# Kernel optimization log

Hardware: AMD Instinct MI355X
Metric: run time of the kernel (lower is better)

## Reference

```python
import jax, jax.numpy as jnp
import numpy as np

# ---- static config ----
H, W = 60, 60
WS = 7          # window size (square)
SS = 3          # shift size
DIM = 256
NH = 8
HD = DIM // NH
N = WS * WS     # tokens per window = 49
HP = (H // WS + 1) * WS  # 63 (padded, matches __init__ mask construction)
WP = (W // WS + 1) * WS  # 63
NW = (HP // WS) * (WP // WS)  # 81 windows
EPS = 1e-5


def _rel_pos_index():
    coords = np.stack(np.meshgrid(np.arange(WS), np.arange(WS), indexing='ij'))  # (2,WS,WS)
    cf = coords.reshape(2, -1)                      # (2, N)
    rel = cf[:, :, None] - cf[:, None, :]           # (2, N, N)
    rel = rel.transpose(1, 2, 0).astype(np.int64)   # (N, N, 2)
    rel[..., 0] += WS - 1
    rel[..., 1] += WS - 1
    rel[..., 0] *= 2 * WS - 1
    return rel.sum(-1)                              # (N, N) in [0, 169)


def _attn_mask():
    img = np.zeros((HP, WP), dtype=np.float32)
    cnt = 0
    for hs in (slice(0, -WS), slice(-WS, -SS), slice(-SS, None)):
        for ws_ in (slice(0, -WS), slice(-WS, -SS), slice(-SS, None)):
            img[hs, ws_] = cnt
            cnt += 1
    mw = img.reshape(HP // WS, WS, WP // WS, WS).transpose(0, 2, 1, 3).reshape(-1, N)  # (NW, N)
    diff = mw[:, None, :] - mw[:, :, None]          # (NW, N, N)
    return np.where(diff != 0, -100.0, 0.0).astype(np.float32)


REL_IDX = _rel_pos_index()
ATTN_MASK = _attn_mask()


def layer_norm(x, g, b):
    mu = jnp.mean(x, axis=-1, keepdims=True)
    var = jnp.mean(jnp.square(x - mu), axis=-1, keepdims=True)
    return (x - mu) * jax.lax.rsqrt(var + EPS) * g + b


def setup_inputs() -> dict:
    key = jax.random.key(0)
    ks = jax.random.split(key, 8)
    B = 24
    std = 0.02
    return {
        'x': jax.random.normal(ks[0], (B, H * W, DIM), jnp.float32),
        'g1': jnp.ones((DIM,), jnp.float32),
        'b1': jnp.zeros((DIM,), jnp.float32),
        'w_qkv': jax.random.normal(ks[1], (DIM, 3 * DIM), jnp.float32) * std,
        'b_qkv': jnp.zeros((3 * DIM,), jnp.float32),
        'rel_bias_table': jax.random.normal(ks[2], ((2 * WS - 1) ** 2, NH), jnp.float32) * std,
        'w_proj': jax.random.normal(ks[3], (DIM, DIM), jnp.float32) * std,
        'b_proj': jnp.zeros((DIM,), jnp.float32),
        'g2': jnp.ones((DIM,), jnp.float32),
        'b2': jnp.zeros((DIM,), jnp.float32),
        'w_fc1': jax.random.normal(ks[4], (DIM, 4 * DIM), jnp.float32) * std,
        'b_fc1': jnp.zeros((4 * DIM,), jnp.float32),
        'w_fc2': jax.random.normal(ks[5], (4 * DIM, DIM), jnp.float32) * std,
        'b_fc2': jnp.zeros((DIM,), jnp.float32),
    }


def _swin_block(x, g1, b1, w_qkv, b_qkv, rel_bias_table, w_proj, b_proj,
                g2, b2, w_fc1, b_fc1, w_fc2, b_fc2):
    B, L, C = x.shape
    shortcut = x
    x = layer_norm(x, g1, b1).reshape(B, H, W, C)
    # pad to (HP, WP)
    x = jnp.pad(x, ((0, 0), (0, HP - H), (0, WP - W), (0, 0)))
    # cyclic shift
    x = jnp.roll(x, (-SS, -SS), axis=(1, 2))
    # window partition -> (B*NW, N, C)
    xw = x.reshape(B, HP // WS, WS, WP // WS, WS, C).transpose(0, 1, 3, 2, 4, 5)
    xw = xw.reshape(B * NW, N, C)
    # attention
    qkv = (xw @ w_qkv + b_qkv).reshape(B * NW, N, 3, NH, HD).transpose(2, 0, 3, 1, 4)
    q, k, v = qkv[0], qkv[1], qkv[2]            # (B*NW, NH, N, HD)
    q = q * (HD ** -0.5)
    attn = jnp.einsum('whnd,whmd->whnm', q, k)  # (B*NW, NH, N, N)
    rel_bias = rel_bias_table[jnp.asarray(REL_IDX)]          # (N, N, NH)
    attn = attn + rel_bias.transpose(2, 0, 1)[None]
    mask = jnp.asarray(ATTN_MASK)                            # (NW, N, N)
    attn = attn.reshape(B, NW, NH, N, N) + mask[None, :, None]
    attn = jax.nn.softmax(attn.reshape(B * NW, NH, N, N), axis=-1)
    out = jnp.einsum('whnm,whmd->whnd', attn, v)             # (B*NW, NH, N, HD)
    out = out.transpose(0, 2, 1, 3).reshape(B * NW, N, C)
    out = out @ w_proj + b_proj
    # window reverse -> (B, HP, WP, C)
    out = out.reshape(B, HP // WS, WP // WS, WS, WS, C).transpose(0, 1, 3, 2, 4, 5)
    out = out.reshape(B, HP, WP, C)
    # reverse shift, unpad
    out = jnp.roll(out, (SS, SS), axis=(1, 2))[:, :H, :W, :].reshape(B, L, C)
    x = shortcut + out
    # MLP
    y = layer_norm(x, g2, b2)
    y = jax.nn.gelu(y @ w_fc1 + b_fc1, approximate=False) @ w_fc2 + b_fc2
    return x + y


def reference(x, g1, b1, w_qkv, b_qkv, rel_bias_table, w_proj, b_proj,
              g2, b2, w_fc1, b_fc1, w_fc2, b_fc2):
    return _swin_block(x, g1, b1, w_qkv, b_qkv, rel_bias_table, w_proj, b_proj,
                       g2, b2, w_fc1, b_fc1, w_fc2, b_fc2)
```

## Files before the change

kernel.cpp:

```cpp
#include <hip/hip_runtime.h>
#include <hip/hip_bf16.h>
#include <math.h>


typedef _Float16 half8 __attribute__((ext_vector_type(8)));
typedef _Float16 half4_t __attribute__((ext_vector_type(4)));
typedef float f32x4 __attribute__((ext_vector_type(4)));

#define GLDS16(gp, lp)                                                    \
  __builtin_amdgcn_global_load_lds(                                      \
      (__attribute__((address_space(1))) const void*)(gp),               \
      (__attribute__((address_space(3))) void*)(lp), 16, 0, 0)

__device__ __forceinline__ float wave_reduce_sum(float v) {
  v += __shfl_xor(v, 1);
  v += __shfl_xor(v, 2);
  v += __shfl_xor(v, 4);
  v += __shfl_xor(v, 8);
  v += __shfl_xor(v, 16);
  v += __shfl_xor(v, 32);
  return v;
}

__global__ __launch_bounds__(256) void prep_weights(
    const float* __restrict__ wqkv, const float* __restrict__ wproj,
    const float* __restrict__ wfc1, const float* __restrict__ wfc2,
    _Float16* __restrict__ oqkv, _Float16* __restrict__ oproj,
    _Float16* __restrict__ ofc1, _Float16* __restrict__ ofc2)
{
  int idx = blockIdx.x * 256 + threadIdx.x;
  if (idx < 196608) {
    int n = idx / 256, k = idx % 256;
    oqkv[idx] = (_Float16)wqkv[k * 768 + n];
  } else if (idx < 262144) {
    int i = idx - 196608; int n = i / 256, k = i % 256;
    oproj[i] = (_Float16)wproj[k * 256 + n];
  } else if (idx < 524288) {
    int i = idx - 262144; int n = i / 256, k = i % 256;
    ofc1[i] = (_Float16)wfc1[k * 1024 + n];
  } else {
    int i = idx - 524288; int n = i / 1024, k = i % 1024;
    ofc2[i] = (_Float16)wfc2[k * 256 + n];
  }
}

__global__ __launch_bounds__(256) void prep_cb(
    const float* __restrict__ rbt, _Float16* __restrict__ cbt)
{
  int idx = blockIdx.x * 256 + threadIdx.x;
  int m = idx & 63, n = (idx >> 6) & 63;
  int hc = idx >> 12; int h = hc & 7, c = hc >> 3;
  float v;
  if (n < 49 && m < 49) {
    int i1 = n / 7, j1 = n % 7, i2 = m / 7, j2 = m % 7;
    float bias = rbt[((i1 - i2 + 6) * 13 + (j1 - j2 + 6)) * 8 + h];
    int rh1 = (c & 2) ? (i1 < 4 ? 1 : 2) : 0;
    int rh2 = (c & 2) ? (i2 < 4 ? 1 : 2) : 0;
    int rw1 = (c & 1) ? (j1 < 4 ? 1 : 2) : 0;
    int rw2 = (c & 1) ? (j2 < 4 ? 1 : 2) : 0;
    v = bias + (((rh1 != rh2) || (rw1 != rw2)) ? -100.f : 0.f);
  } else {
    v = -60000.f;
  }
  cbt[idx] = (_Float16)v;
}

__global__ __launch_bounds__(256) void ln1_window_kernel(
    const float* __restrict__ x, const float* __restrict__ g,
    const float* __restrict__ bta, _Float16* __restrict__ xw,
    int row0, int rows_c)
{
  int lrow = blockIdx.x * 4 + (threadIdx.x >> 6);
  if (lrow >= rows_c) return;
  int row = row0 + lrow;
  int lane = threadIdx.x & 63;
  int bw = row / 49, n = row - bw * 49;
  int b = bw / 81, win = bw - b * 81;
  int wh = win / 9, ww = win - wh * 9;
  int i = n / 7, j = n - i * 7;
  int sh = wh * 7 + i + 3; if (sh >= 63) sh -= 63;
  int sw = ww * 7 + j + 3; if (sw >= 63) sw -= 63;
  bool valid = (sh < 60) && (sw < 60);
  float4 v = make_float4(0.f, 0.f, 0.f, 0.f);
  if (valid)
    v = reinterpret_cast<const float4*>(x + ((size_t)b * 3600 + sh * 60 + sw) * 256)[lane];
  float s = v.x + v.y + v.z + v.w;
  s = wave_reduce_sum(s);
  float mu = s * (1.f / 256.f);
  float dx = v.x - mu, dy = v.y - mu, dz = v.z - mu, dw = v.w - mu;
  float q = dx * dx + dy * dy + dz * dz + dw * dw;
  q = wave_reduce_sum(q);
  float rs = rsqrtf(q * (1.f / 256.f) + 1e-5f);
  float4 gv = reinterpret_cast<const float4*>(g)[lane];
  float4 bv = reinterpret_cast<const float4*>(bta)[lane];
  union { _Float16 h[4]; uint2 u; } pk;
  if (valid) {
    pk.h[0] = (_Float16)(dx * rs * gv.x + bv.x);
    pk.h[1] = (_Float16)(dy * rs * gv.y + bv.y);
    pk.h[2] = (_Float16)(dz * rs * gv.z + bv.z);
    pk.h[3] = (_Float16)(dw * rs * gv.w + bv.w);
  } else {
    pk.h[0] = pk.h[1] = pk.h[2] = pk.h[3] = (_Float16)0.f;
  }
  *reinterpret_cast<uint2*>(xw + (size_t)lrow * 256 + lane * 4) = pk.u;
}

__global__ __launch_bounds__(256, 2) void gemm_kernel(
    const _Float16* __restrict__ A, const _Float16* __restrict__ Bt,
    const float* __restrict__ bias, const float* __restrict__ resid,
    void* __restrict__ out, int M, int N, int K, int mode, int row0)
{
  __shared__ __align__(16) _Float16 lds[2][2][8192];
  const int tid = threadIdx.x;
  const int n0 = blockIdx.x * 128, m0 = blockIdx.y * 128;
  const int wv = tid >> 6, ln = tid & 63;
  const int wm = (wv >> 1) * 64, wn = (wv & 1) * 64;
  const int quad = ln >> 4, l16 = ln & 15;

  const int rl = ln >> 3;
  const int gseg = ((ln & 7) ^ rl) << 3;
  const _Float16* gA[4]; const _Float16* gB[4];
#pragma unroll
  for (int s = 0; s < 4; s++) {
    int r = wv * 32 + s * 8 + rl;
    int gm = m0 + r; if (gm >= M) gm = M - 1;
    gA[s] = A + (size_t)gm * K + gseg;
    gB[s] = Bt + (size_t)(n0 + r) * K + gseg;
  }

  int offA[2][4], offB[2][4];
#pragma unroll
  for (int i = 0; i < 4; i++) {
    int ra = wm + i * 16 + l16;
    int rb = wn + i * 16 + l16;
    int sw0 = l16 & 7;
#pragma unroll
    for (int ks = 0; ks < 2; ks++) {
      offA[ks][i] = ra * 64 + (((ks * 4 + quad) ^ sw0) << 3);
      offB[ks][i] = rb * 64 + (((ks * 4 + quad) ^ sw0) << 3);
    }
  }

  f32x4 acc[4][4];
#pragma unroll
  for (int i = 0; i < 4; i++)
#pragma unroll
    for (int j = 0; j < 4; j++) acc[i][j] = (f32x4)0.f;

#define STAGE(buf, koff)                                                   \
  {                                                                        \
    _Float16* la = &lds[buf][0][wv * 2048];                                \
    _Float16* lb = &lds[buf][1][wv * 2048];                                \
    GLDS16(gA[0] + (koff), la);        GLDS16(gB[0] + (koff), lb);         \
    GLDS16(gA[1] + (koff), la + 512);  GLDS16(gB[1] + (koff), lb + 512);   \
    GLDS16(gA[2] + (koff), la + 1024); GLDS16(gB[2] + (koff), lb + 1024);  \
    GLDS16(gA[3] + (koff), la + 1536); GLDS16(gB[3] + (koff), lb + 1536);  \
  }

  const int nt = K >> 6;
  STAGE(0, 0);
  __syncthreads();
  for (int t = 0; t < nt; t++) {
    const int cur = t & 1;
    half8 a0[4], b0[4], a1[4], b1[4];
#pragma unroll
    for (int i = 0; i < 4; i++) {
      a0[i] = *reinterpret_cast<const half8*>(&lds[cur][0][offA[0][i]]);
      a1[i] = *reinterpret_cast<const half8*>(&lds[cur][0][offA[1][i]]);
      b0[i] = *reinterpret_cast<const half8*>(&lds[cur][1][offB[0][i]]);
      b1[i] = *reinterpret_cast<const half8*>(&lds[cur][1][offB[1][i]]);
    }
    if (t + 1 < nt) STAGE(cur ^ 1, (t + 1) << 6);
#pragma unroll
    for (int i = 0; i < 4; i++)
#pragma unroll
      for (int j = 0; j < 4; j++)
        acc[i][j] = __builtin_amdgcn_mfma_f32_16x16x32_f16(b0[j], a0[i], acc[i][j], 0, 0, 0);
#pragma unroll
    for (int i = 0; i < 4; i++)
#pragma unroll
      for (int j = 0; j < 4; j++)
        acc[i][j] = __builtin_amdgcn_mfma_f32_16x16x32_f16(b1[j], a1[i], acc[i][j], 0, 0, 0);
    __syncthreads();
  }
#undef STAGE

  f32x4 bias4[4];
#pragma unroll
  for (int j = 0; j < 4; j++)
    bias4[j] = *reinterpret_cast<const f32x4*>(bias + n0 + wn + j * 16 + quad * 4);

#pragma unroll
  for (int i = 0; i < 4; i++) {
    int gm = m0 + wm + i * 16 + l16;
    if (gm >= M) continue;
    if (mode == 0) {
      _Float16* op = reinterpret_cast<_Float16*>(out) + (size_t)gm * N + n0 + wn;
#pragma unroll
      for (int j = 0; j < 4; j++) {
        float sc = (n0 + wn + j * 16) < 256 ? 0.17677669529663687f : 1.f;
        half4_t o4;
#pragma unroll
        for (int r = 0; r < 4; r++)
          o4[r] = (_Float16)((acc[i][j][r] + bias4[j][r]) * sc);
        *reinterpret_cast<half4_t*>(op + j * 16 + quad * 4) = o4;
      }
    } else {
      int gmg = gm + row0;
      int bw = gmg / 49, nn = gmg - bw * 49;
      int bidx = bw / 81, win = bw - bidx * 81;
      int wh = win / 9, wwn = win - wh * 9;
      int ii = nn / 7, jj = nn - ii * 7;
      int sh = wh * 7 + ii + 3; if (sh >= 63) sh -= 63;
      int sw = wwn * 7 + jj + 3; if (sw >= 63) sw -= 63;
      if (sh < 60 && sw < 60) {
        size_t o = ((size_t)bidx * 3600 + sh * 60 + sw) * 256 + n0 + wn;
        float* op = reinterpret_cast<float*>(out) + o;
        const float* rp = resid + o;
#pragma unroll
        for (int j = 0; j < 4; j++) {
          f32x4 rv = *reinterpret_cast<const f32x4*>(rp + j * 16 + quad * 4);
          f32x4 v = acc[i][j] + bias4[j] + rv;
          *reinterpret_cast<f32x4*>(op + j * 16 + quad * 4) = v;
        }
      }
    }
  }
}

__global__ __launch_bounds__(256, 1) void fused_mlp_kernel(
    const float* __restrict__ X, const _Float16* __restrict__ W1t,
    const float* __restrict__ B1v, const _Float16* __restrict__ W2t,
    const float* __restrict__ B2v, const float* __restrict__ g,
    const float* __restrict__ bt, float* __restrict__ out, int M)
{
  __shared__ __align__(16) _Float16 Alds[128 * 256];
  __shared__ __align__(16) _Float16 Hlds[128 * 128];
  const int tid = threadIdx.x;
  const int wv = tid >> 6, ln = tid & 63;
  const int quad = ln >> 4, l16 = ln & 15;
  const int m0 = blockIdx.x * 128;
  const int wm = (wv >> 1) * 64;
  const int wn = (wv & 1) * 64;
  const int wn2 = (wv & 1) * 128;

  {
    float4 gv = reinterpret_cast<const float4*>(g)[ln];
    float4 bv = reinterpret_cast<const float4*>(bt)[ln];
    int seg = ln >> 1;
    for (int rr = 0; rr < 32; rr++) {
      int lr = wv * 32 + rr;
      int gr = m0 + lr; if (gr >= M) gr = M - 1;
      float4 v = reinterpret_cast<const float4*>(X + (size_t)gr * 256)[ln];
      float s = wave_reduce_sum(v.x + v.y + v.z + v.w);
      float mu = s * (1.f / 256.f);
      float dx = v.x - mu, dy = v.y - mu, dz = v.z - mu, dw = v.w - mu;
      float q = wave_reduce_sum(dx * dx + dy * dy + dz * dz + dw * dw);
      float rs = rsqrtf(q * (1.f / 256.f) + 1e-5f);
      union { _Float16 h[4]; uint2 u; } pk;
      pk.h[0] = (_Float16)(dx * rs * gv.x + bv.x);
      pk.h[1] = (_Float16)(dy * rs * gv.y + bv.y);
      pk.h[2] = (_Float16)(dz * rs * gv.z + bv.z);
      pk.h[3] = (_Float16)(dw * rs * gv.w + bv.w);
      *reinterpret_cast<uint2*>(
          &Alds[lr * 256 + ((seg ^ (lr & 31)) << 3) + (ln & 1) * 4]) = pk.u;
    }
  }

  f32x4 acc[4][8];
  {
    f32x4 b2q[8];
#pragma unroll
    for (int j = 0; j < 8; j++)
      b2q[j] = *reinterpret_cast<const f32x4*>(B2v + wn2 + j * 16 + quad * 4);
#pragma unroll
    for (int i = 0; i < 4; i++) {
      int gr = m0 + wm + i * 16 + l16; if (gr >= M) gr = M - 1;
      const float* xp = X + (size_t)gr * 256 + wn2;
#pragma unroll
      for (int j = 0; j < 8; j++)
        acc[i][j] = *reinterpret_cast<const f32x4*>(xp + j * 16 + quad * 4) + b2q[j];
    }
  }
  __syncthreads();

  for (int n1 = 0; n1 < 8; n1++) {
    f32x4 acch[4][4];
#pragma unroll
    for (int i = 0; i < 4; i++)
#pragma unroll
      for (int j = 0; j < 4; j++) acch[i][j] = (f32x4)0.f;
    for (int t = 0; t < 4; t++) {
#pragma unroll
      for (int ks = 0; ks < 2; ks++) {
        half8 bf[4], af[4];
#pragma unroll
        for (int j = 0; j < 4; j++)
          bf[j] = *reinterpret_cast<const half8*>(
              W1t + (size_t)(n1 * 128 + wn + j * 16 + l16) * 256 + t * 64 + ks * 32 + quad * 8);
#pragma unroll
        for (int i = 0; i < 4; i++) {
          int ra = wm + i * 16 + l16;
          af[i] = *reinterpret_cast<const half8*>(
              &Alds[ra * 256 + (((t * 8 + ks * 4 + quad) ^ (ra & 31)) << 3)]);
        }
#pragma unroll
        for (int i = 0; i < 4; i++)
#pragma unroll
          for (int j = 0; j < 4; j++)
            acch[i][j] = __builtin_amdgcn_mfma_f32_16x16x32_f16(bf[j], af[i], acch[i][j], 0, 0, 0);
      }
    }
    __syncthreads();
    {
      f32x4 b1q[4];
#pragma unroll
      for (int j = 0; j < 4; j++)
        b1q[j] = *reinterpret_cast<const f32x4*>(B1v + n1 * 128 + wn + j * 16 + quad * 4);
#pragma unroll
      for (int i = 0; i < 4; i++) {
        int mrow = wm + i * 16 + l16;
#pragma unroll
        for (int j = 0; j < 4; j++) {
          int c = wn + j * 16 + quad * 4;
          half4_t o4;
#pragma unroll
          for (int r = 0; r < 4; r++) {
            float v = acch[i][j][r] + b1q[j][r];
            v = 0.5f * v * (1.f + erff(v * 0.70710678118654752f));
            o4[r] = (_Float16)v;
          }
          *reinterpret_cast<half4_t*>(
              &Hlds[mrow * 128 + (((c >> 3) ^ (mrow & 15)) << 3) + (quad & 1) * 4]) = o4;
        }
      }
    }
    __syncthreads();
#pragma unroll
    for (int t2 = 0; t2 < 2; t2++) {
#pragma unroll
      for (int ks = 0; ks < 2; ks++) {
        half8 hf[4], b2f[8];
#pragma unroll
        for (int i = 0; i < 4; i++) {
          int mh = wm + i * 16 + l16;
          hf[i] = *reinterpret_cast<const half8*>(
              &Hlds[mh * 128 + (((t2 * 8 + ks * 4 + quad) ^ (mh & 15)) << 3)]);
        }
#pragma unroll
        for (int j = 0; j < 8; j++)
          b2f[j] = *reinterpret_cast<const half8*>(
              W2t + (size_t)(wn2 + j * 16 + l16) * 1024 + n1 * 128 + t2 * 64 + ks * 32 + quad * 8);
#pragma unroll
        for (int i = 0; i < 4; i++)
#pragma unroll
          for (int j = 0; j < 8; j++)
            acc[i][j] = __builtin_amdgcn_mfma_f32_16x16x32_f16(b2f[j], hf[i], acc[i][j], 0, 0, 0);
      }
    }
  }

#pragma unroll
  for (int i = 0; i < 4; i++) {
    int gm = m0 + wm + i * 16 + l16;
    if (gm >= M) continue;
    float* op = out + (size_t)gm * 256 + wn2;
#pragma unroll
    for (int j = 0; j < 8; j++)
      *reinterpret_cast<f32x4*>(op + j * 16 + quad * 4) = acc[i][j];
  }
}

__global__ __launch_bounds__(64) void attn_mfma(
    const _Float16* __restrict__ qkv, const _Float16* __restrict__ cbt,
    _Float16* __restrict__ outp)
{
  __shared__ __align__(16) _Float16 VT[32][72];
  __shared__ __align__(16) _Float16 Ps[64][72];
  const int bwh = blockIdx.x;
  const int bw = bwh >> 3, h = bwh & 7;
  const int win = bw % 81;
  const int wh = win / 9, ww = win - wh * 9;
  const int cls = ((wh == 8) ? 2 : 0) | ((ww == 8) ? 1 : 0);
  const int lane = threadIdx.x;
  const int quad = lane >> 4, l16 = lane & 15;

  for (int e = lane; e < 480; e += 64) {
    int d = e / 15, m = 49 + e % 15;
    VT[d][m] = (_Float16)0.f;
  }
  const size_t vbase = (size_t)bw * 49 * 768 + 512 + h * 32;
  for (int e = lane; e < 1568; e += 64) {
    int m = e >> 5, d = e & 31;
    VT[d][m] = qkv[vbase + (size_t)m * 768 + d];
  }

  const _Float16* qb = qkv + (size_t)bw * 49 * 768 + h * 32 + quad * 8;
  half8 kf[4], qf[4];
  const half8 hz = (half8)(_Float16)0.f;
#pragma unroll
  for (int t = 0; t < 4; t++) {
    int row = t * 16 + l16;
    int rc = row < 49 ? row : 48;
    half8 kv = *reinterpret_cast<const half8*>(qb + 256 + (size_t)rc * 768);
    half8 qv = *reinterpret_cast<const half8*>(qb + (size_t)rc * 768);
    kf[t] = row < 49 ? kv : hz;
    qf[t] = row < 49 ? qv : hz;
  }

  f32x4 S[4][4];
#pragma unroll
  for (int mt = 0; mt < 4; mt++)
#pragma unroll
    for (int nt = 0; nt < 4; nt++) S[mt][nt] = (f32x4)0.f;
#pragma unroll
  for (int mt = 0; mt < 4; mt++)
#pragma unroll
    for (int nt = 0; nt < 4; nt++)
      S[mt][nt] = __builtin_amdgcn_mfma_f32_16x16x32_f16(kf[mt], qf[nt], S[mt][nt], 0, 0, 0);

  const _Float16* cbp = cbt + (((size_t)cls * 8 + h) << 12);
#pragma unroll
  for (int nt = 0; nt < 4; nt++) {
    int n = nt * 16 + l16;
#pragma unroll
    for (int mt = 0; mt < 4; mt++) {
      half4_t cb4 = *reinterpret_cast<const half4_t*>(cbp + n * 64 + mt * 16 + quad * 4);
#pragma unroll
      for (int r = 0; r < 4; r++) S[mt][nt][r] += (float)cb4[r];
    }
  }

  float inv[4];
#pragma unroll
  for (int nt = 0; nt < 4; nt++) {
    float mx = -3.0e38f;
#pragma unroll
    for (int mt = 0; mt < 4; mt++)
#pragma unroll
      for (int r = 0; r < 4; r++) mx = fmaxf(mx, S[mt][nt][r]);
    mx = fmaxf(mx, __shfl_xor(mx, 16));
    mx = fmaxf(mx, __shfl_xor(mx, 32));
    float sm = 0.f;
#pragma unroll
    for (int mt = 0; mt < 4; mt++)
#pragma unroll
      for (int r = 0; r < 4; r++) {
        float e = __expf(S[mt][nt][r] - mx);
        S[mt][nt][r] = e;
        sm += e;
      }
    sm += __shfl_xor(sm, 16);
    sm += __shfl_xor(sm, 32);
    inv[nt] = 1.f / sm;
  }

#pragma unroll
  for (int nt = 0; nt < 4; nt++) {
#pragma unroll
    for (int mt = 0; mt < 4; mt++) {
      half4_t p;
#pragma unroll
      for (int r = 0; r < 4; r++) p[r] = (_Float16)(S[mt][nt][r] * inv[nt]);
      *reinterpret_cast<half4_t*>(&Ps[nt * 16 + l16][mt * 16 + quad * 4]) = p;
    }
  }
  __syncthreads();

  f32x4 O[2][4];
#pragma unroll
  for (int dt = 0; dt < 2; dt++)
#pragma unroll
    for (int nt = 0; nt < 4; nt++) O[dt][nt] = (f32x4)0.f;
#pragma unroll
  for (int ks = 0; ks < 2; ks++) {
    half8 va[2], pb[4];
#pragma unroll
    for (int dt = 0; dt < 2; dt++)
      va[dt] = *reinterpret_cast<const half8*>(&VT[dt * 16 + l16][ks * 32 + quad * 8]);
#pragma unroll
    for (int nt = 0; nt < 4; nt++)
      pb[nt] = *reinterpret_cast<const half8*>(&Ps[nt * 16 + l16][ks * 32 + quad * 8]);
#pragma unroll
    for (int dt = 0; dt < 2; dt++)
#pragma unroll
      for (int nt = 0; nt < 4; nt++)
        O[dt][nt] = __builtin_amdgcn_mfma_f32_16x16x32_f16(va[dt], pb[nt], O[dt][nt], 0, 0, 0);
  }

#pragma unroll
  for (int nt = 0; nt < 4; nt++) {
    int n = nt * 16 + l16;
    if (n < 49) {
#pragma unroll
      for (int dt = 0; dt < 2; dt++) {
        half4_t o4;
#pragma unroll
        for (int r = 0; r < 4; r++) o4[r] = (_Float16)O[dt][nt][r];
        *reinterpret_cast<half4_t*>(
            outp + ((size_t)bw * 49 + n) * 256 + h * 32 + dt * 16 + quad * 4) = o4;
      }
    }
  }
}

extern "C" void kernel_launch(void* const* d_in, const int* in_sizes, int n_in,
                              void* d_out, int out_size, void* d_ws, size_t ws_size,
                              hipStream_t stream) {
  const float* x      = (const float*)d_in[0];
  const float* g1     = (const float*)d_in[1];
  const float* b1     = (const float*)d_in[2];
  const float* w_qkv  = (const float*)d_in[3];
  const float* b_qkv  = (const float*)d_in[4];
  const float* rbt    = (const float*)d_in[5];
  const float* w_proj = (const float*)d_in[6];
  const float* b_proj = (const float*)d_in[7];
  const float* g2     = (const float*)d_in[8];
  const float* b2     = (const float*)d_in[9];
  const float* w_fc1  = (const float*)d_in[10];
  const float* b_fc1  = (const float*)d_in[11];
  const float* w_fc2  = (const float*)d_in[12];
  const float* b_fc2  = (const float*)d_in[13];
  float* outp = (float*)d_out;

  char* ws = (char*)d_ws;
  _Float16* wqkvT  = (_Float16*)(ws + 0);
  _Float16* wprojT = (_Float16*)(ws + 393216);
  _Float16* wfc1T  = (_Float16*)(ws + 524288);
  _Float16* wfc2T  = (_Float16*)(ws + 1048576);
  _Float16* cbt    = (_Float16*)(ws + 1572864);
  const size_t WB = 1835008;

  const int cand[8] = {24, 12, 8, 6, 4, 3, 2, 1};
  int cb = 1;
  for (int ci = 0; ci < 8; ci++) {
    size_t need = WB + (size_t)cand[ci] * (2032128u + 6096384u);
    if (ws_size >= need) { cb = cand[ci]; break; }
  }
  const int nch = 24 / cb;

  _Float16* r1 = (_Float16*)(ws + WB);
  _Float16* r2 = (_Float16*)(ws + WB + (size_t)cb * 2032128u);

  prep_weights<<<3072, 256, 0, stream>>>(w_qkv, w_proj, w_fc1, w_fc2,
                                         wqkvT, wprojT, wfc1T, wfc2T);
  prep_cb<<<512, 256, 0, stream>>>(rbt, cbt);

  for (int c = 0; c < nch; c++) {
    const int b0 = c * cb;
    const int rows_att = cb * 81 * 49;
    const int row0_att = b0 * 81 * 49;
    const int rows_mlp = cb * 3600;
    const int row0_mlp = b0 * 3600;

    ln1_window_kernel<<<(rows_att + 3) / 4, 256, 0, stream>>>(
        x, g1, b1, r1, row0_att, rows_att);
    {
      dim3 g(6, (rows_att + 127) / 128);
      gemm_kernel<<<g, 256, 0, stream>>>(r1, wqkvT, b_qkv, nullptr, r2,
                                         rows_att, 768, 256, 0, 0);
    }
    attn_mfma<<<cb * 81 * 8, 64, 0, stream>>>(r2, cbt, r1);
    {
      dim3 g(2, (rows_att + 127) / 128);
      gemm_kernel<<<g, 256, 0, stream>>>(r1, wprojT, b_proj, x, outp,
                                         rows_att, 256, 256, 1, row0_att);
    }
    {
      float* od = outp + (size_t)row0_mlp * 256;
      fused_mlp_kernel<<<(rows_mlp + 127) / 128, 256, 0, stream>>>(
          od, wfc1T, b_fc1, wfc2T, b_fc2, g2, b2, od, rows_mlp);
    }
  }
}
```

Before: 753.9 us.

## Shrink fused MLP row tile to 64 and double-buffer hidden LDS tile

The fused LayerNorm+MLP kernel now processes 64 rows per block instead of 128. Each of the four waves owns a 32-column slice of the hidden chunk and a 64-column slice of the output. The hidden activation buffer is double-buffered, which removes one __syncthreads per chunk, and smaller LDS and register use allow two blocks per CU (launch bounds 256,2). The trade-off is that each block reloads W1/W2 fragments from global memory for half as many rows, so weight traffic per output row doubles, in exchange for more occupancy and more blocks.

```diff
diff --git a/kernel.cpp b/kernel.cpp
--- a/kernel.cpp
+++ b/kernel.cpp
@@ -228,28 +228,27 @@
   }
 }
 
-__global__ __launch_bounds__(256, 1) void fused_mlp_kernel(
+__global__ __launch_bounds__(256, 2) void fused_mlp_kernel(
     const float* __restrict__ X, const _Float16* __restrict__ W1t,
     const float* __restrict__ B1v, const _Float16* __restrict__ W2t,
     const float* __restrict__ B2v, const float* __restrict__ g,
     const float* __restrict__ bt, float* __restrict__ out, int M)
 {
-  __shared__ __align__(16) _Float16 Alds[128 * 256];
-  __shared__ __align__(16) _Float16 Hlds[128 * 128];
+  __shared__ __align__(16) _Float16 Alds[64 * 256];
+  __shared__ __align__(16) _Float16 Hlds[2][64 * 128];
   const int tid = threadIdx.x;
   const int wv = tid >> 6, ln = tid & 63;
   const int quad = ln >> 4, l16 = ln & 15;
-  const int m0 = blockIdx.x * 128;
-  const int wm = (wv >> 1) * 64;
-  const int wn = (wv & 1) * 64;
-  const int wn2 = (wv & 1) * 128;
+  const int m0 = blockIdx.x * 64;
+  const int wn1 = wv * 32;
+  const int wn2 = wv * 64;
 
   {
     float4 gv = reinterpret_cast<const float4*>(g)[ln];
     float4 bv = reinterpret_cast<const float4*>(bt)[ln];
-    int seg = ln >> 1;
-    for (int rr = 0; rr < 32; rr++) {
-      int lr = wv * 32 + rr;
+    const int seg = ln >> 1;
+    for (int rr = 0; rr < 16; rr++) {
+      int lr = wv * 16 + rr;
       int gr = m0 + lr; if (gr >= M) gr = M - 1;
       float4 v = reinterpret_cast<const float4*>(X + (size_t)gr * 256)[ln];
       float s = wave_reduce_sum(v.x + v.y + v.z + v.w);
@@ -267,62 +266,61 @@
     }
   }
 
-  f32x4 acc[4][8];
+  f32x4 acc[4][4];
   {
-    f32x4 b2q[8];
-#pragma unroll
-    for (int j = 0; j < 8; j++)
+    f32x4 b2q[4];
+#pragma unroll
+    for (int j = 0; j < 4; j++)
       b2q[j] = *reinterpret_cast<const f32x4*>(B2v + wn2 + j * 16 + quad * 4);
 #pragma unroll
     for (int i = 0; i < 4; i++) {
-      int gr = m0 + wm + i * 16 + l16; if (gr >= M) gr = M - 1;
+      int gr = m0 + i * 16 + l16; if (gr >= M) gr = M - 1;
       const float* xp = X + (size_t)gr * 256 + wn2;
 #pragma unroll
-      for (int j = 0; j < 8; j++)
+      for (int j = 0; j < 4; j++)
         acc[i][j] = *reinterpret_cast<const f32x4*>(xp + j * 16 + quad * 4) + b2q[j];
     }
   }
   __syncthreads();
 
-  for (int n1 = 0; n1 < 8; n1++) {
-    f32x4 acch[4][4];
+  for (int n1c = 0; n1c < 8; n1c++) {
+    f32x4 acch[4][2];
 #pragma unroll
     for (int i = 0; i < 4; i++)
 #pragma unroll
-      for (int j = 0; j < 4; j++) acch[i][j] = (f32x4)0.f;
-    for (int t = 0; t < 4; t++) {
-#pragma unroll
-      for (int ks = 0; ks < 2; ks++) {
-        half8 bf[4], af[4];
-#pragma unroll
-        for (int j = 0; j < 4; j++)
-          bf[j] = *reinterpret_cast<const half8*>(
-              W1t + (size_t)(n1 * 128 + wn + j * 16 + l16) * 256 + t * 64 + ks * 32 + quad * 8);
-#pragma unroll
-        for (int i = 0; i < 4; i++) {
-          int ra = wm + i * 16 + l16;
-          af[i] = *reinterpret_cast<const half8*>(
-              &Alds[ra * 256 + (((t * 8 + ks * 4 + quad) ^ (ra & 31)) << 3)]);
-        }
-#pragma unroll
-        for (int i = 0; i < 4; i++)
-#pragma unroll
-          for (int j = 0; j < 4; j++)
-            acch[i][j] = __builtin_amdgcn_mfma_f32_16x16x32_f16(bf[j], af[i], acch[i][j], 0, 0, 0);
-      }
-    }
-    __syncthreads();
+      for (int j = 0; j < 2; j++) acch[i][j] = (f32x4)0.f;
+    const _Float16* w1p = W1t + (size_t)(n1c * 128 + wn1) * 256;
+#pragma unroll
+    for (int st = 0; st < 8; st++) {
+      half8 bf[2], af[4];
+#pragma unroll
+      for (int j = 0; j < 2; j++)
+        bf[j] = *reinterpret_cast<const half8*>(
+            w1p + (size_t)(j * 16 + l16) * 256 + st * 32 + quad * 8);
+#pragma unroll
+      for (int i = 0; i < 4; i++) {
+        int ra = i * 16 + l16;
+        af[i] = *reinterpret_cast<const half8*>(
+            &Alds[ra * 256 + (((st * 4 + quad) ^ (ra & 31)) << 3)]);
+      }
+#pragma unroll
+      for (int i = 0; i < 4; i++)
+#pragma unroll
+        for (int j = 0; j < 2; j++)
+          acch[i][j] = __builtin_amdgcn_mfma_f32_16x16x32_f16(bf[j], af[i], acch[i][j], 0, 0, 0);
+    }
+    _Float16* hb = &Hlds[n1c & 1][0];
     {
-      f32x4 b1q[4];
-#pragma unroll
-      for (int j = 0; j < 4; j++)
-        b1q[j] = *reinterpret_cast<const f32x4*>(B1v + n1 * 128 + wn + j * 16 + quad * 4);
+      f32x4 b1q[2];
+#pragma unroll
+      for (int j = 0; j < 2; j++)
+        b1q[j] = *reinterpret_cast<const f32x4*>(B1v + n1c * 128 + wn1 + j * 16 + quad * 4);
 #pragma unroll
       for (int i = 0; i < 4; i++) {
-        int mrow = wm + i * 16 + l16;
-#pragma unroll
-        for (int j = 0; j < 4; j++) {
-          int c = wn + j * 16 + quad * 4;
+        int m = i * 16 + l16;
+#pragma unroll
+        for (int j = 0; j < 2; j++) {
+          int n = wn1 + j * 16 + quad * 4;
           half4_t o4;
 #pragma unroll
           for (int r = 0; r < 4; r++) {
@@ -331,42 +329,40 @@
             o4[r] = (_Float16)v;
           }
           *reinterpret_cast<half4_t*>(
-              &Hlds[mrow * 128 + (((c >> 3) ^ (mrow & 15)) << 3) + (quad & 1) * 4]) = o4;
+              &hb[m * 128 + (((n >> 3) ^ (m & 15)) << 3) + (quad & 1) * 4]) = o4;
         }
       }
     }
     __syncthreads();
-#pragma unroll
-    for (int t2 = 0; t2 < 2; t2++) {
-#pragma unroll
-      for (int ks = 0; ks < 2; ks++) {
-        half8 hf[4], b2f[8];
-#pragma unroll
-        for (int i = 0; i < 4; i++) {
-          int mh = wm + i * 16 + l16;
-          hf[i] = *reinterpret_cast<const half8*>(
-              &Hlds[mh * 128 + (((t2 * 8 + ks * 4 + quad) ^ (mh & 15)) << 3)]);
-        }
-#pragma unroll
-        for (int j = 0; j < 8; j++)
-          b2f[j] = *reinterpret_cast<const half8*>(
-              W2t + (size_t)(wn2 + j * 16 + l16) * 1024 + n1 * 128 + t2 * 64 + ks * 32 + quad * 8);
-#pragma unroll
-        for (int i = 0; i < 4; i++)
-#pragma unroll
-          for (int j = 0; j < 8; j++)
-            acc[i][j] = __builtin_amdgcn_mfma_f32_16x16x32_f16(b2f[j], hf[i], acc[i][j], 0, 0, 0);
-      }
+    const _Float16* w2p = W2t + (size_t)wn2 * 1024 + n1c * 128;
+#pragma unroll
+    for (int p = 0; p < 4; p++) {
+      half8 hf[4], b2f[4];
+#pragma unroll
+      for (int j = 0; j < 4; j++)
+        b2f[j] = *reinterpret_cast<const half8*>(
+            w2p + (size_t)(j * 16 + l16) * 1024 + p * 32 + quad * 8);
+#pragma unroll
+      for (int i = 0; i < 4; i++) {
+        int mh = i * 16 + l16;
+        hf[i] = *reinterpret_cast<const half8*>(
+            &hb[mh * 128 + (((p * 4 + quad) ^ (mh & 15)) << 3)]);
+      }
+#pragma unroll
+      for (int i = 0; i < 4; i++)
+#pragma unroll
+        for (int j = 0; j < 4; j++)
+          acc[i][j] = __builtin_amdgcn_mfma_f32_16x16x32_f16(b2f[j], hf[i], acc[i][j], 0, 0, 0);
     }
   }
 
 #pragma unroll
   for (int i = 0; i < 4; i++) {
-    int gm = m0 + wm + i * 16 + l16;
+    int gm = m0 + i * 16 + l16;
     if (gm >= M) continue;
     float* op = out + (size_t)gm * 256 + wn2;
 #pragma unroll
-    for (int j = 0; j < 8; j++)
+    for (int j = 0; j < 4; j++)
       *reinterpret_cast<f32x4*>(op + j * 16 + quad * 4) = acc[i][j];
   }
 }
@@ -568,7 +564,7 @@
     }
     {
       float* od = outp + (size_t)row0_mlp * 256;
-      fused_mlp_kernel<<<(rows_mlp + 127) / 128, 256, 0, stream>>>(
+      fused_mlp_kernel<<<(rows_mlp + 63) / 64, 256, 0, stream>>>(
           od, wfc1T, b_fc1, wfc2T, b_fc2, g2, b2, od, rows_mlp);
     }
   }
```

Measured after the change: 653.1 us. -13.4%, faster.
